# Optimization experiments

Hardware: AMD Instinct MI355X
Metric: run time of the kernel (lower is better)

## Reference

```python
import jax, jax.numpy as jnp
import numpy as np

EPS = 1e-7  # K.epsilon()
ROUTINGS = 3
NUM_CAPSULE = 32
DIM_CAPSULE = 64

def _squash(x, axis=-1):
    # NOTE: this repo's 'squash' is just L2-ish normalization: x / sqrt(||x||^2 + eps)
    s2 = jnp.sum(jnp.square(x), axis=axis, keepdims=True)
    return x / jnp.sqrt(s2 + EPS)

def setup_inputs() -> dict:
    key = jax.random.key(0)
    k1, k2 = jax.random.split(key)
    u_vecs = jax.random.normal(k1, (32, 1024, 256), dtype=jnp.float32)
    # shared-weight capsule kernel: (1, input_dim_capsule, num_capsule*dim_capsule)
    W = jax.random.normal(k2, (1, 256, NUM_CAPSULE * DIM_CAPSULE), dtype=jnp.float32) * 0.05
    return {"u_vecs": u_vecs, "W": W}

def reference(u_vecs, W):
    B, N, D = u_vecs.shape
    # conv1d with width-1 kernel == matmul over feature dim
    u_hat = jnp.einsum('bnd,dm->bnm', u_vecs, W[0])          # [B, N, NC*DC]
    u_hat = u_hat.reshape(B, N, NUM_CAPSULE, DIM_CAPSULE)
    u_hat = jnp.transpose(u_hat, (0, 2, 1, 3))               # [B, NC, N, DC]

    b = jnp.zeros((B, NUM_CAPSULE, N), dtype=u_hat.dtype)    # routing logits
    v = None
    for i in range(ROUTINGS):
        c = jax.nn.softmax(b, axis=-1)                       # over input capsules
        s = jnp.einsum('bij,bijd->bid', c, u_hat)            # weighted sum
        v = _squash(s)                                       # [B, NC, DC]
        if i < ROUTINGS - 1:
            b = b + jnp.einsum('bid,bijd->bij', v, u_hat)    # agreement update
    return v
```

## Files before the change

### kernel.cpp

```cpp
#include <hip/hip_runtime.h>
#include <math.h>


typedef short v8s __attribute__((ext_vector_type(8)));
typedef short v4s __attribute__((ext_vector_type(4)));
typedef float v4f __attribute__((ext_vector_type(4)));

__device__ __forceinline__ unsigned short f2bf(float x) {
    unsigned u = __float_as_uint(x);
    u = u + 0x7fffu + ((u >> 16) & 1u);
    return (unsigned short)(u >> 16);
}
__device__ __forceinline__ float bf2f(unsigned short h) {
    return __uint_as_float(((unsigned)h) << 16);
}

__global__ __launch_bounds__(256) void k_init(const float* __restrict__ U,
                                              const float* __restrict__ W,
                                              float* __restrict__ t0p,
                                              float* __restrict__ WT,
                                              short* __restrict__ Ubf) {
    int bid = blockIdx.x, tid = threadIdx.x;
    if (bid < 512) {
        int b = bid >> 4, q = bid & 15;
        int row0 = (b << 10) + (q << 6);
        const float* Up = U + (row0 << 8) + tid;
        short* Ub = Ubf + (row0 << 8) + tid;
        float acc = 0.f;
        #pragma unroll 8
        for (int jl = 0; jl < 64; ++jl) {
            float x = Up[jl << 8];
            acc += x;
            Ub[jl << 8] = (short)f2bf(x);
        }
        t0p[(b << 12) + (q << 8) + tid] = acc * (1.0f / 1024.0f);
    } else {
        __shared__ float tile[64 * 65];
        int tix = bid - 512;
        int k0 = (tix >> 5) << 6, c0 = (tix & 31) << 6;
        int cc = tid & 63, g4 = tid >> 6;
        #pragma unroll
        for (int r = 0; r < 16; ++r) {
            int kk = (g4 << 4) + r;
            tile[kk * 65 + cc] = W[(k0 + kk) * 2048 + c0 + cc];
        }
        __syncthreads();
        int kk = tid & 63;
        #pragma unroll
        for (int r = 0; r < 16; ++r) {
            int c = (g4 << 4) + r;
            WT[(c0 + c) * 256 + k0 + kk] = tile[kk * 65 + c];
        }
    }
}

__global__ __launch_bounds__(256) void k_sv(const float* __restrict__ t0p,
                                            float* __restrict__ t,
                                            float* __restrict__ sef,
                                            const float* __restrict__ W,
                                            const float* __restrict__ WT,
                                            short* __restrict__ wbt_h,
                                            short* __restrict__ wbt_l,
                                            float* __restrict__ out,
                                            int mode, int writeOut) {
    __shared__ float t_lds[256];
    __shared__ float spart[256];
    __shared__ __align__(16) float v_lds[64];
    __shared__ __align__(16) v4f spartw[256];
    __shared__ float sefv_s;
    int bid = blockIdx.x, tid = threadIdx.x;
    int b = bid >> 5, iG = bid & 31;
    int bg = (b << 1) | (iG >> 4), il = iG & 15;
    int row = (bg << 4) + il;

    float acc;
    if (mode == 0) {
        const float* tb = t0p + (b << 12) + tid;
        acc = 0.f;
        #pragma unroll
        for (int q = 0; q < 16; ++q) acc += tb[q << 8];
        if (tid == 0) sefv_s = 1.0f;
        t[(row << 8) + tid] = 0.f;
        if (tid == 0) sef[row] = 0.f;
    } else {
        acc = t[(row << 8) + tid];
        if (tid == 0) sefv_s = sef[row];
        if (!writeOut) {
            t[(row << 8) + tid] = 0.f;
            if (tid == 0) sef[row] = 0.f;
        }
    }
    t_lds[tid] = acc;
    __syncthreads();

    int d = tid & 63, kq = tid >> 6;
    const float* Wc = W + ((kq << 6) * 2048) + (iG << 6) + d;
    float s = 0.f;
    #pragma unroll 4
    for (int kk = 0; kk < 64; ++kk)
        s += t_lds[(kq << 6) + kk] * Wc[kk * 2048];
    spart[tid] = s;
    __syncthreads();

    if (tid < 64) {
        float sv = spart[tid] + spart[tid + 64] + spart[tid + 128] + spart[tid + 192];
        float n2 = sv * sv;
        #pragma unroll
        for (int m = 1; m < 64; m <<= 1) n2 += __shfl_xor(n2, m, 64);
        float sf = sefv_s;
        float v = sv * rsqrtf(n2 + 1e-7f * sf * sf);
        v_lds[tid] = v;
        if (writeOut) out[(bid << 6) + tid] = v;
    }
    __syncthreads();
    if (writeOut) return;

    int k4 = tid & 63, dq = tid >> 6;
    const float4* WT4 = (const float4*)WT;
    v4f wp = {0.f, 0.f, 0.f, 0.f};
    #pragma unroll
    for (int dd = 0; dd < 16; ++dd) {
        float vv = v_lds[(dq << 4) + dd];
        float4 wt = WT4[((iG << 6) + (dq << 4) + dd) * 64 + k4];
        wp.x += vv * wt.x; wp.y += vv * wt.y; wp.z += vv * wt.z; wp.w += vv * wt.w;
    }
    spartw[(dq << 6) + k4] = wp;
    __syncthreads();
    if (tid < 64) {
        v4f w = spartw[tid] + spartw[64 + tid] + spartw[128 + tid] + spartw[192 + tid];
        float wv4[4] = {w.x, w.y, w.z, w.w};
        unsigned short wh[4], wl[4];
        #pragma unroll
        for (int e = 0; e < 4; ++e) {
            wh[e] = f2bf(wv4[e]);
            wl[e] = f2bf(wv4[e] - bf2f(wh[e]));
        }
        int base = (row << 8) + (tid << 2);
        *(v4s*)&wbt_h[base] = (v4s){(short)wh[0], (short)wh[1], (short)wh[2], (short)wh[3]};
        *(v4s*)&wbt_l[base] = (v4s){(short)wl[0], (short)wl[1], (short)wl[2], (short)wl[3]};
    }
}

__global__ __launch_bounds__(1024, 8) void k_pass(const short* __restrict__ Ubf,
                                                  const short* __restrict__ wbt_h,
                                                  const short* __restrict__ wbt_l,
                                                  float* __restrict__ bmatg,
                                                  float* __restrict__ t,
                                                  float* __restrict__ sef,
                                                  int addold) {
    __shared__ short s_U[64 * 268];
    __shared__ short s_wh[16 * 264];
    __shared__ short s_wl[16 * 264];
    __shared__ short s_eh[16 * 72];
    __shared__ short s_el[16 * 72];
    __shared__ float s_red[16 * 320];
    __shared__ float s_sefp[16 * 16];

    const int tid = threadIdx.x, wv = tid >> 6, lane = tid & 63;
    const int quad = lane >> 4, nn = lane & 15;
    const int blk = blockIdx.x;
    const int b = blk & 31, pg = blk >> 5;
    const int p = pg >> 1, g2 = pg & 1;
    const int bg = (b << 1) | g2;
    const int rowbase = (b << 10) + (p << 6);

    const int mt2 = wv & 3, jq = wv >> 2;
    const int rr = (jq << 2) + quad;
    const int jloc = (mt2 << 4) + rr;
    const int ga = (((bg << 10) + (p << 6) + jloc) << 4) + nn;
    float bold = 0.f;
    if (addold) bold = bmatg[ga];

    if (tid < 512) {
        int row = tid >> 5, seg = tid & 31;
        int gidx = (((bg << 4) + row) << 8) + (seg << 3);
        *(v8s*)&s_wh[row * 264 + (seg << 3)] = *(const v8s*)(wbt_h + gidx);
        *(v8s*)&s_wl[row * 264 + (seg << 3)] = *(const v8s*)(wbt_l + gidx);
    }
    {
        const short* Ub = Ubf + (rowbase << 8);
        int col = tid & 31, row0 = tid >> 5;
        v8s u0 = *(const v8s*)(Ub + (row0 << 8) + (col << 3));
        v8s u1 = *(const v8s*)(Ub + ((row0 + 32) << 8) + (col << 3));
        *(v4s*)&s_U[row0 * 268 + (col << 3)]            = __builtin_shufflevector(u0, u0, 0, 1, 2, 3);
        *(v4s*)&s_U[row0 * 268 + (col << 3) + 4]        = __builtin_shufflevector(u0, u0, 4, 5, 6, 7);
        *(v4s*)&s_U[(row0 + 32) * 268 + (col << 3)]     = __builtin_shufflevector(u1, u1, 0, 1, 2, 3);
        *(v4s*)&s_U[(row0 + 32) * 268 + (col << 3) + 4] = __builtin_shufflevector(u1, u1, 4, 5, 6, 7);
    }
    __syncthreads();

    {
        const int mt = wv & 3, kq = wv >> 2;
        v4f dacc = {0.f, 0.f, 0.f, 0.f};
        #pragma unroll
        for (int c = 0; c < 2; ++c) {
            int kb = (kq << 6) + (c << 5) + (quad << 3);
            v8s a  = *(const v8s*)&s_U[((mt << 4) + nn) * 268 + kb];
            v8s bh = *(const v8s*)&s_wh[nn * 264 + kb];
            v8s bl = *(const v8s*)&s_wl[nn * 264 + kb];
            dacc = __builtin_amdgcn_mfma_f32_16x16x32_bf16(a, bh, dacc, 0, 0, 0);
            dacc = __builtin_amdgcn_mfma_f32_16x16x32_bf16(a, bl, dacc, 0, 0, 0);
        }
        #pragma unroll
        for (int r = 0; r < 4; ++r)
            s_red[wv * 320 + ((quad << 2) + r) * 20 + nn] = dacc[r];
    }
    __syncthreads();

    {
        float val = bold;
        #pragma unroll
        for (int kq = 0; kq < 4; ++kq)
            val += s_red[((kq << 2) + mt2) * 320 + rr * 20 + nn];
        if (!addold) bmatg[ga] = val;
        float e = __expf(val);
        unsigned short eh = f2bf(e);
        s_eh[nn * 72 + jloc] = (short)eh;
        s_el[nn * 72 + jloc] = (short)f2bf(e - bf2f(eh));
        float se = e;
        se += __shfl_xor(se, 16, 64);
        se += __shfl_xor(se, 32, 64);
        if (lane < 16) s_sefp[(wv << 4) + lane] = se;
    }
    __syncthreads();

    {
        v4f tacc = {0.f, 0.f, 0.f, 0.f};
        const int k0 = wv << 4;
        #pragma unroll
        for (int jc = 0; jc < 2; ++jc) {
            v8s aeh = *(const v8s*)&s_eh[nn * 72 + (jc << 5) + (quad << 3)];
            v8s ael = *(const v8s*)&s_el[nn * 72 + (jc << 5) + (quad << 3)];
            short bu[8];
            #pragma unroll
            for (int jj = 0; jj < 8; ++jj)
                bu[jj] = s_U[((jc << 5) + (quad << 3) + jj) * 268 + k0 + nn];
            v8s bf = (v8s){bu[0], bu[1], bu[2], bu[3], bu[4], bu[5], bu[6], bu[7]};
            tacc = __builtin_amdgcn_mfma_f32_16x16x32_bf16(aeh, bf, tacc, 0, 0, 0);
            tacc = __builtin_amdgcn_mfma_f32_16x16x32_bf16(ael, bf, tacc, 0, 0, 0);
        }
        #pragma unroll
        for (int r = 0; r < 4; ++r) {
            int i = (quad << 2) + r;
            unsafeAtomicAdd(&t[(((bg << 4) + i) << 8) + k0 + nn], tacc[r]);
        }
    }
    if (tid < 16) {
        float ss = 0.f;
        #pragma unroll
        for (int w = 0; w < 16; ++w) ss += s_sefp[(w << 4) + tid];
        unsafeAtomicAdd(&sef[(bg << 4) + tid], ss);
    }
}

extern "C" void kernel_launch(void* const* d_in, const int* in_sizes, int n_in,
                              void* d_out, int out_size, void* d_ws, size_t ws_size,
                              hipStream_t stream) {
    const float* U = (const float*)d_in[0];
    const float* W = (const float*)d_in[1];
    float* out = (float*)d_out;
    float* ws = (float*)d_ws;

    float* t0p   = ws;
    float* WT    = t0p + 131072;
    float* bmatg = WT + 524288;
    float* t     = bmatg + 1048576;
    float* sef   = t + 262144;
    short* wbt_h = (short*)(sef + 1024);
    short* wbt_l = wbt_h + 262144;
    short* Ubf   = wbt_l + 262144;

    k_init<<<640, 256, 0, stream>>>(U, W, t0p, WT, Ubf);
    k_sv<<<1024, 256, 0, stream>>>(t0p, t, sef, W, WT,
                                   wbt_h, wbt_l, out, 0, 0);
    k_pass<<<1024, 1024, 0, stream>>>(Ubf, wbt_h, wbt_l, bmatg, t, sef, 0);
    k_sv<<<1024, 256, 0, stream>>>(t0p, t, sef, W, WT,
                                   wbt_h, wbt_l, out, 1, 0);
    k_pass<<<1024, 1024, 0, stream>>>(Ubf, wbt_h, wbt_l, bmatg, t, sef, 1);
    k_sv<<<1024, 256, 0, stream>>>(t0p, t, sef, W, WT,
                                   wbt_h, wbt_l, out, 1, 1);
}
```

Baseline: 137.3 us.

## Fuse squash/projection step into routing pass via last-block atomic counter

Removes the separate k_sv launches after each routing pass. Each k_pass block increments a per-batch-group counter, and the last of the 16 blocks reads the accumulated t and sef, computes v, then writes either the output or the next bf16 hi/lo projected weights. This cuts two kernel launches and their global round-trips. In exchange the serial tail runs on only 64 blocks, each doing a 256-long dot loop per wave, and it adds a fence plus atomic ordering.

After: 213.0 us. 55.1% more time.

```diff
diff --git a/kernel.cpp b/kernel.cpp
--- a/kernel.cpp
+++ b/kernel.cpp
@@ -54,42 +54,30 @@
     }
 }
 
-__global__ __launch_bounds__(256) void k_sv(const float* __restrict__ t0p,
-                                            float* __restrict__ t,
-                                            float* __restrict__ sef,
-                                            const float* __restrict__ W,
-                                            const float* __restrict__ WT,
-                                            short* __restrict__ wbt_h,
-                                            short* __restrict__ wbt_l,
-                                            float* __restrict__ out,
-                                            int mode, int writeOut) {
+__global__ __launch_bounds__(256) void k_sv0(const float* __restrict__ t0p,
+                                             float* __restrict__ t,
+                                             float* __restrict__ sef,
+                                             int* __restrict__ ctr,
+                                             const float* __restrict__ W,
+                                             const float* __restrict__ WT,
+                                             short* __restrict__ wbt_h,
+                                             short* __restrict__ wbt_l) {
     __shared__ float t_lds[256];
     __shared__ float spart[256];
     __shared__ __align__(16) float v_lds[64];
     __shared__ __align__(16) v4f spartw[256];
-    __shared__ float sefv_s;
     int bid = blockIdx.x, tid = threadIdx.x;
     int b = bid >> 5, iG = bid & 31;
     int bg = (b << 1) | (iG >> 4), il = iG & 15;
     int row = (bg << 4) + il;
 
-    float acc;
-    if (mode == 0) {
-        const float* tb = t0p + (b << 12) + tid;
-        acc = 0.f;
-        #pragma unroll
-        for (int q = 0; q < 16; ++q) acc += tb[q << 8];
-        if (tid == 0) sefv_s = 1.0f;
-        t[(row << 8) + tid] = 0.f;
-        if (tid == 0) sef[row] = 0.f;
-    } else {
-        acc = t[(row << 8) + tid];
-        if (tid == 0) sefv_s = sef[row];
-        if (!writeOut) {
-            t[(row << 8) + tid] = 0.f;
-            if (tid == 0) sef[row] = 0.f;
-        }
-    }
+    const float* tb = t0p + (b << 12) + tid;
+    float acc = 0.f;
+    #pragma unroll
+    for (int q = 0; q < 16; ++q) acc += tb[q << 8];
+    t[(row << 8) + tid] = 0.f;
+    if (tid == 0) sef[row] = 0.f;
+    if (tid == 0 && il == 0) ctr[bg] = 0;
     t_lds[tid] = acc;
     __syncthreads();
 
@@ -107,13 +95,10 @@
         float n2 = sv * sv;
         #pragma unroll
         for (int m = 1; m < 64; m <<= 1) n2 += __shfl_xor(n2, m, 64);
-        float sf = sefv_s;
-        float v = sv * rsqrtf(n2 + 1e-7f * sf * sf);
+        float v = sv * rsqrtf(n2 + 1e-7f);
         v_lds[tid] = v;
-        if (writeOut) out[(bid << 6) + tid] = v;
-    }
-    __syncthreads();
-    if (writeOut) return;
+    }
+    __syncthreads();
 
     int k4 = tid & 63, dq = tid >> 6;
     const float4* WT4 = (const float4*)WT;
@@ -147,7 +132,11 @@
                                                   float* __restrict__ bmatg,
                                                   float* __restrict__ t,
                                                   float* __restrict__ sef,
-                                                  int addold) {
+                                                  int* __restrict__ ctr,
+                                                  const float* __restrict__ W,
+                                                  const float* __restrict__ WT,
+                                                  float* __restrict__ out,
+                                                  int addold, int writeOut) {
     __shared__ short s_U[64 * 268];
     __shared__ short s_wh[16 * 264];
     __shared__ short s_wl[16 * 264];
@@ -155,6 +144,7 @@
     __shared__ short s_el[16 * 72];
     __shared__ float s_red[16 * 320];
     __shared__ float s_sefp[16 * 16];
+    __shared__ int s_last;
 
     const int tid = threadIdx.x, wv = tid >> 6, lane = tid & 63;
     const int quad = lane >> 4, nn = lane & 15;
@@ -251,6 +241,66 @@
         for (int w = 0; w < 16; ++w) ss += s_sefp[(w << 4) + tid];
         unsafeAtomicAdd(&sef[(bg << 4) + tid], ss);
     }
+
+    __syncthreads();
+    if (tid == 0) {
+        __threadfence();
+        int old = __hip_atomic_fetch_add(&ctr[bg], 1, __ATOMIC_ACQ_REL,
+                                         __HIP_MEMORY_SCOPE_AGENT);
+        s_last = (old == 15);
+        if (old == 15) ctr[bg] = 0;
+    }
+    __syncthreads();
+    if (!s_last) return;
+
+    float* t_l = (float*)s_red;
+    #pragma unroll
+    for (int r = 0; r < 4; ++r) {
+        int o = (r << 10) + tid;
+        float xv = __hip_atomic_load(&t[(bg << 12) + o], __ATOMIC_RELAXED,
+                                     __HIP_MEMORY_SCOPE_AGENT);
+        t_l[o] = xv;
+        if (!writeOut) t[(bg << 12) + o] = 0.f;
+    }
+    float sefv = __hip_atomic_load(&sef[(bg << 4) + wv], __ATOMIC_RELAXED,
+                                   __HIP_MEMORY_SCOPE_AGENT);
+    if (!writeOut && tid < 16) sef[(bg << 4) + tid] = 0.f;
+    __syncthreads();
+
+    const int il = wv, iGt = ((bg & 1) << 4) | il;
+    const float* Wc = W + iGt * 64 + lane;
+    float sv = 0.f;
+    #pragma unroll 8
+    for (int kk = 0; kk < 256; ++kk)
+        sv += t_l[(il << 8) + kk] * Wc[kk * 2048];
+    float n2 = sv * sv;
+    #pragma unroll
+    for (int m = 1; m < 64; m <<= 1) n2 += __shfl_xor(n2, m, 64);
+    float vv = sv * rsqrtf(n2 + 1e-7f * sefv * sefv);
+
+    if (writeOut) {
+        out[((bg >> 1) << 11) + (iGt << 6) + lane] = vv;
+        return;
+    }
+
+    const float4* WT4 = (const float4*)WT;
+    v4f wp = {0.f, 0.f, 0.f, 0.f};
+    #pragma unroll 8
+    for (int dd = 0; dd < 64; ++dd) {
+        float vd = __shfl(vv, dd, 64);
+        float4 wt = WT4[((iGt << 6) + dd) * 64 + lane];
+        wp.x += vd * wt.x; wp.y += vd * wt.y; wp.z += vd * wt.z; wp.w += vd * wt.w;
+    }
+    unsigned short wh[4], wl[4];
+    float wv4[4] = {wp.x, wp.y, wp.z, wp.w};
+    #pragma unroll
+    for (int e = 0; e < 4; ++e) {
+        wh[e] = f2bf(wv4[e]);
+        wl[e] = f2bf(wv4[e] - bf2f(wh[e]));
+    }
+    int base = (((bg << 4) + il) << 8) + (lane << 2);
+    *(v4s*)&((short*)wbt_h)[base] = (v4s){(short)wh[0], (short)wh[1], (short)wh[2], (short)wh[3]};
+    *(v4s*)&((short*)wbt_l)[base] = (v4s){(short)wl[0], (short)wl[1], (short)wl[2], (short)wl[3]};
 }
 
 extern "C" void kernel_launch(void* const* d_in, const int* in_sizes, int n_in,
@@ -269,14 +319,13 @@
     short* wbt_h = (short*)(sef + 1024);
     short* wbt_l = wbt_h + 262144;
     short* Ubf   = wbt_l + 262144;
+    int*   ctr   = (int*)(Ubf + 8388608);
 
     k_init<<<640, 256, 0, stream>>>(U, W, t0p, WT, Ubf);
-    k_sv<<<1024, 256, 0, stream>>>(t0p, t, sef, W, WT,
-                                   wbt_h, wbt_l, out, 0, 0);
-    k_pass<<<1024, 1024, 0, stream>>>(Ubf, wbt_h, wbt_l, bmatg, t, sef, 0);
-    k_sv<<<1024, 256, 0, stream>>>(t0p, t, sef, W, WT,
-                                   wbt_h, wbt_l, out, 1, 0);
-    k_pass<<<1024, 1024, 0, stream>>>(Ubf, wbt_h, wbt_l, bmatg, t, sef, 1);
-    k_sv<<<1024, 256, 0, stream>>>(t0p, t, sef, W, WT,
-                                   wbt_h, wbt_l, out, 1, 1);
-}
+    k_sv0<<<1024, 256, 0, stream>>>(t0p, t, sef, ctr, W, WT, wbt_h, wbt_l);
+    k_pass<<<1024, 1024, 0, stream>>>((const short*)wbt_h == nullptr ? nullptr : Ubf,
+                                      wbt_h, wbt_l, bmatg, t, sef, ctr,
+                                      W, WT, out, 0, 0);
+    k_pass<<<1024, 1024, 0, stream>>>(Ubf, wbt_h, wbt_l, bmatg, t, sef, ctr,
+                                      W, WT, out, 1, 1);
+}
```
